# Kernel tuning notes

Measured on AMD Instinct MI355X. Metric: run time of the kernel, lower is better.

The kernel has to match this reference:

```python
import jax, jax.numpy as jnp
import numpy as np

B, T, D = 16, 4096, 256
CODEBOOK_SIZE = 1024
COMMITMENT = 1.0


def setup_inputs() -> dict:
    key = jax.random.key(0)
    kx, kc = jax.random.split(key)
    x = jax.random.normal(kx, (B, T, D), dtype=jnp.float32)
    codebook = jax.random.normal(kc, (CODEBOOK_SIZE, D), dtype=jnp.float32)
    return {"x": x, "codebook": codebook}


def reference(x, codebook):
    # x: [B, T, D] continuous latents; codebook: [K, D]
    flat = x.reshape(-1, x.shape[-1])  # [N, D]
    # does not affect argmin but is kept for faithfulness to torch.cdist-style math)
    x_sq = jnp.sum(flat * flat, axis=1, keepdims=True)            # [N, 1]
    c_sq = jnp.sum(codebook * codebook, axis=1)                   # [K]
    dist = x_sq - 2.0 * (flat @ codebook.T) + c_sq[None, :]       # [N, K]
    indices = jnp.argmin(dist, axis=1)                            # [N] int
    quantized = codebook[indices].reshape(x.shape)                # gather, [B, T, D]
    # commitment loss: encoder pulled toward (stopped) codes
    commit_loss = COMMITMENT * jnp.mean(
        (x - jax.lax.stop_gradient(quantized)) ** 2
    )
    # straight-through estimator
    out = x + jax.lax.stop_gradient(quantized - x)
    return out, indices.reshape(x.shape[:-1]), commit_loss
```

## Files before the change

kernel.cpp:

```cpp
#include <hip/hip_runtime.h>

#define N_TOK 65536
#define DIM   256
#define KCODE 1024

#define NTHREADS 256
#define TM 128
#define TN 128
#define BK 64
#define NCHUNK 8

#define REFINE_EPS 0.125f
#define TIE_THETA 1.0e-4

#define WS_CSQ_OFF   16
#define WS_IDX_OFF   2048
#define WS_PAIRS_OFF (WS_IDX_OFF + N_TOK)
#define WS_CBPK_OFF  (WS_PAIRS_OFF + N_TOK * NCHUNK * 4)

typedef float f32x4  __attribute__((ext_vector_type(4)));
typedef short bf16x8 __attribute__((ext_vector_type(8)));

__global__ void zero_loss_kernel(float* ws) {
    if (threadIdx.x == 0) ws[0] = 0.0f;
}

__global__ void rowsq_np_kernel(const float* __restrict__ m,
                                float* __restrict__ out, int rows) {
#pragma clang fp contract(off)
    int row = blockIdx.x * 16 + (threadIdx.x >> 4);
    int l   = threadIdx.x & 15;
    if (row >= rows) return;
    int h = l >> 3;
    int j = l & 7;
    const float* p = m + (size_t)row * DIM + h * 128 + j;
    float v = p[0];
    float r = v * v;
#pragma unroll
    for (int i = 1; i < 16; ++i) {
        float w  = p[i * 8];
        float w2 = w * w;
        r = r + w2;
    }
    float t = r + __shfl_xor(r, 1);
    t = t + __shfl_xor(t, 2);
    t = t + __shfl_xor(t, 4);
    t = t + __shfl_xor(t, 8);
    if (l == 0) out[row] = t;
}

__device__ __forceinline__ void ins2(float d, int idx,
                                     float& d1, int& i1, float& d2, int& i2) {
    if (d < d1 || (d == d1 && idx < i1)) {
        d2 = d1; i2 = i1; d1 = d; i1 = idx;
    } else if ((d < d2 || (d == d2 && idx < i2)) && idx != i1) {
        d2 = d; i2 = idx;
    }
}

__device__ __forceinline__ void f2bf_split(float v, short& hi, short& lo) {
    unsigned u = __float_as_uint(v);
    unsigned r = (u + 0x7fffu + ((u >> 16) & 1u)) >> 16;
    hi = (short)r;
    float hf = __uint_as_float(r << 16);
    float lf = v - hf;
    unsigned u2 = __float_as_uint(lf);
    unsigned r2 = (u2 + 0x7fffu + ((u2 >> 16) & 1u)) >> 16;
    lo = (short)r2;
}

__global__ void convert_pack_kernel(const float* __restrict__ src,
                                    unsigned short* __restrict__ dst,
                                    int nquads) {
    for (int i = blockIdx.x * blockDim.x + threadIdx.x; i < nquads;
         i += gridDim.x * blockDim.x) {
        int row = i >> 6;
        int kq  = i & 63;
        float4 v = reinterpret_cast<const float4*>(src)[i];
        short h0, l0, h1, l1, h2, l2, h3, l3;
        f2bf_split(v.x, h0, l0); f2bf_split(v.y, h1, l1);
        f2bf_split(v.z, h2, l2); f2bf_split(v.w, h3, l3);
        *reinterpret_cast<short4*>(dst + (size_t)row * 512 + kq * 4) =
            make_short4(h0, h1, h2, h3);
        *reinterpret_cast<short4*>(dst + (size_t)row * 512 + 256 + kq * 4) =
            make_short4(l0, l1, l2, l3);
    }
}

__device__ __forceinline__ void gload_lds16(const unsigned short* g, unsigned short* lds) {
    __builtin_amdgcn_global_load_lds(
        (const __attribute__((address_space(1))) unsigned int*)g,
        (__attribute__((address_space(3))) unsigned int*)lds, 16, 0, 0);
}

__launch_bounds__(NTHREADS, 2)
__global__ void vq_main_kernel(const unsigned short* __restrict__ xpk,
                               const unsigned short* __restrict__ cbpk,
                               const float* __restrict__ csq,
                               float4* __restrict__ pairs) {
    __shared__ __align__(16) unsigned short shbuf[2][TM * BK + TN * BK];

    const int tid  = threadIdx.x;
    const int w    = tid >> 6;
    const int wy   = w >> 1;
    const int wx   = w & 1;
    const int lane = tid & 63;
    const int lm   = lane & 15;
    const int q    = lane >> 4;

    const int bx     = blockIdx.x;
    const int jj     = bx >> 3;
    const int grp    = (bx & 7) + ((jj >> 3) << 3);
    const int cchunk = jj & 7;
    const int tok0   = grp * TM;
    const int code0  = cchunk * TN;

    const int row_off = lane >> 3;
    const int slot    = lane & 7;
    const int kq      = slot ^ row_off;

    float cs_reg[4];
#pragma unroll
    for (int ni = 0; ni < 4; ++ni)
        cs_reg[ni] = csq[code0 + wx * 64 + ni * 16 + lm];

    f32x4 acc[4][4];
#pragma unroll
    for (int mi = 0; mi < 4; ++mi)
#pragma unroll
        for (int ni = 0; ni < 4; ++ni)
            acc[mi][ni] = (f32x4){0.f, 0.f, 0.f, 0.f};

    auto stage = [&](int p, int s) {
        const int seg = s >> 2;
        const int k0  = (s & 3) * BK;
        const int sa  = (seg == 2) ? 256 : 0;
        const int sb  = (seg == 1) ? 256 : 0;
        unsigned short* At = &shbuf[p][0];
        unsigned short* Bt = &shbuf[p][TM * BK];
#pragma unroll
        for (int inst = 0; inst < 4; ++inst) {
            int rbase = w * 32 + inst * 8;
            const unsigned short* ga =
                xpk + (size_t)(tok0 + rbase + row_off) * 512 + sa + k0 + kq * 8;
            gload_lds16(ga, &At[rbase * BK]);
            const unsigned short* gb =
                cbpk + (size_t)(code0 + rbase + row_off) * 512 + sb + k0 + kq * 8;
            gload_lds16(gb, &Bt[rbase * BK]);
        }
    };

    stage(0, 0);
    __syncthreads();

    int p = 0;
#pragma unroll 1
    for (int s = 0; s < 12; ++s) {
        if (s < 11) stage(p ^ 1, s + 1);

        const unsigned short* At = &shbuf[p][0];
        const unsigned short* Bt = &shbuf[p][TM * BK];
#pragma unroll
        for (int t = 0; t < 2; ++t) {
            bf16x8 af[4], bf[4];
#pragma unroll
            for (int mi = 0; mi < 4; ++mi) {
                int r = wy * 64 + mi * 16 + lm;
                af[mi] = *reinterpret_cast<const bf16x8*>(
                    &At[r * BK + (((t * 4 + q) ^ (r & 7)) * 8)]);
            }
#pragma unroll
            for (int ni = 0; ni < 4; ++ni) {
                int r = wx * 64 + ni * 16 + lm;
                bf[ni] = *reinterpret_cast<const bf16x8*>(
                    &Bt[r * BK + (((t * 4 + q) ^ (r & 7)) * 8)]);
            }
#pragma unroll
            for (int mi = 0; mi < 4; ++mi)
#pragma unroll
                for (int ni = 0; ni < 4; ++ni)
                    acc[mi][ni] = __builtin_amdgcn_mfma_f32_16x16x32_bf16(
                        af[mi], bf[ni], acc[mi][ni], 0, 0, 0);
        }

        __syncthreads();
        p ^= 1;
    }

    float4 (*pairs_sh)[2] = reinterpret_cast<float4(*)[2]>(&shbuf[0][0]);

#pragma unroll
    for (int mi = 0; mi < 4; ++mi) {
#pragma unroll
        for (int r = 0; r < 4; ++r) {
            int row_local = wy * 64 + mi * 16 + q * 4 + r;
            float l1 = 3.4e38f, l2 = 3.4e38f;
            int   j1 = 0x7fffffff, j2 = 0x7fffffff;
#pragma unroll
            for (int ni = 0; ni < 4; ++ni) {
                float d = cs_reg[ni] - 2.0f * acc[mi][ni][r];
                ins2(d, code0 + wx * 64 + ni * 16 + lm, l1, j1, l2, j2);
            }
#pragma unroll
            for (int m = 1; m < 16; m <<= 1) {
                float o1 = __shfl_xor(l1, m);
                int   p1 = __shfl_xor(j1, m);
                float o2 = __shfl_xor(l2, m);
                int   p2 = __shfl_xor(j2, m);
                ins2(o1, p1, l1, j1, l2, j2);
                ins2(o2, p2, l1, j1, l2, j2);
            }
            if (lm == 0) {
                float4 pr;
                pr.x = l1; pr.y = l2;
                pr.z = __int_as_float(j1); pr.w = __int_as_float(j2);
                pairs_sh[row_local][wx] = pr;
            }
        }
    }
    __syncthreads();
    if (tid < TM) {
        float4 pa = pairs_sh[tid][0];
        float4 pb = pairs_sh[tid][1];
        float d1 = pa.x, d2 = pa.y;
        int   i1 = __float_as_int(pa.z), i2 = __float_as_int(pa.w);
        ins2(pb.x, __float_as_int(pb.z), d1, i1, d2, i2);
        ins2(pb.y, __float_as_int(pb.w), d1, i1, d2, i2);
        float4 pr;
        pr.x = d1; pr.y = d2;
        pr.z = __int_as_float(i1); pr.w = __int_as_float(i2);
        pairs[(size_t)(tok0 + tid) * NCHUNK + cchunk] = pr;
    }
}

__global__ void merge_refine_kernel(const float* __restrict__ x,
                                    const float* __restrict__ cb,
                                    const float4* __restrict__ pairs,
                                    int* __restrict__ idx_out) {
    int t = blockIdx.x * 256 + threadIdx.x;
    if (t >= N_TOK) return;
    float4 p0 = pairs[(size_t)t * NCHUNK];
    float d1 = p0.x, d2 = p0.y;
    int   i1 = __float_as_int(p0.z), i2 = __float_as_int(p0.w);
#pragma unroll
    for (int c = 1; c < NCHUNK; ++c) {
        float4 p = pairs[(size_t)t * NCHUNK + c];
        ins2(p.x, __float_as_int(p.z), d1, i1, d2, i2);
        ins2(p.y, __float_as_int(p.w), d1, i1, d2, i2);
    }

    int pick = i1;
    if (d2 - d1 < REFINE_EPS) {
        const float* xr = x + (size_t)t * DIM;
        const float* c1 = cb + (size_t)i1 * DIM;
        const float* c2 = cb + (size_t)i2 * DIM;
        double sA = 0.0, dA = 0.0, sB = 0.0, dB = 0.0;
        for (int k = 0; k < DIM; ++k) {
            double xv = (double)xr[k];
            double a  = (double)c1[k];
            double b  = (double)c2[k];
            sA += a * a; dA += xv * a;
            sB += b * b; dB += xv * b;
        }
        double DA  = sA - 2.0 * dA;
        double DB  = sB - 2.0 * dB;
        double gap = DB - DA;
        if (gap > TIE_THETA)       pick = i1;
        else if (gap < -TIE_THETA) pick = i2;
        else                       pick = (i1 < i2) ? i1 : i2;
    }
    idx_out[t] = pick;
}

__launch_bounds__(NTHREADS)
__global__ void output_kernel(const float* __restrict__ x,
                              const float* __restrict__ cb,
                              const int* __restrict__ idx,
                              float* __restrict__ out_q,
                              float* __restrict__ out_idx,
                              float* __restrict__ loss_ws) {
    __shared__ int   sh_idx[TM];
    __shared__ float wsum[4];
    const int tid  = threadIdx.x;
    const int tok0 = blockIdx.x * TM;

    if (tid < TM) sh_idx[tid] = idx[tok0 + tid];
    __syncthreads();

    float lsum = 0.0f;
    for (int t = 0; t < TM; ++t) {
        int code = sh_idx[t];
        float qv = cb[(size_t)code * DIM + tid];
        float xv = x[(size_t)(tok0 + t) * DIM + tid];
        out_q[(size_t)(tok0 + t) * DIM + tid] = xv + (qv - xv);
        float df = xv - qv;
        lsum = fmaf(df, df, lsum);
    }
    if (tid < TM) out_idx[tok0 + tid] = (float)sh_idx[tid];

#pragma unroll
    for (int off = 1; off < 64; off <<= 1) lsum += __shfl_xor(lsum, off);
    if ((tid & 63) == 0) wsum[tid >> 6] = lsum;
    __syncthreads();
    if (tid == 0) atomicAdd(loss_ws, (wsum[0] + wsum[1]) + (wsum[2] + wsum[3]));
}

__global__ void finalize_kernel(const float* ws, float* out_loss) {
    if (threadIdx.x == 0) out_loss[0] = ws[0] * (1.0f / 16777216.0f);
}

extern "C" void kernel_launch(void* const* d_in, const int* in_sizes, int n_in,
                              void* d_out, int out_size, void* d_ws, size_t ws_size,
                              hipStream_t stream) {
    const float* x  = (const float*)d_in[0];
    const float* cb = (const float*)d_in[1];

    float* out      = (float*)d_out;
    float* out_q    = out;
    float* out_idx  = out + (size_t)N_TOK * DIM;
    float* out_loss = out_idx + N_TOK;

    float*  ws    = (float*)d_ws;
    float*  csq   = ws + WS_CSQ_OFF;
    int*    idx   = (int*)(ws + WS_IDX_OFF);
    float4* pairs = (float4*)(ws + WS_PAIRS_OFF);
    unsigned short* cbpk = (unsigned short*)(ws + WS_CBPK_OFF);
    unsigned short* xpk  = (unsigned short*)out_q;

    zero_loss_kernel<<<1, 64, 0, stream>>>(ws);
    rowsq_np_kernel<<<KCODE / 16, 256, 0, stream>>>(cb, csq, KCODE);
    convert_pack_kernel<<<4096, 256, 0, stream>>>(x, xpk, N_TOK * (DIM / 4));
    convert_pack_kernel<<<256, 256, 0, stream>>>(cb, cbpk, KCODE * (DIM / 4));
    vq_main_kernel<<<(N_TOK / TM) * NCHUNK, NTHREADS, 0, stream>>>(xpk, cbpk, csq, pairs);
    merge_refine_kernel<<<N_TOK / 256, 256, 0, stream>>>(x, cb, pairs, idx);
    output_kernel<<<N_TOK / TM, NTHREADS, 0, stream>>>(x, cb, idx, out_q, out_idx, ws);
    finalize_kernel<<<1, 64, 0, stream>>>(ws, out_loss);
}
```

Before: 917.5 us.

## Pre-tile packed bf16 operands into swizzled k-chunks and halve LDS tile depth

The pack kernel now writes x and codebook as contiguous pre-swizzled 128x32 tiles (hi and lo halves in separate chunks), so each GEMM stage is a few fully contiguous 16-byte global-to-LDS loads. BK drops from 64 to 32 with 24 stages, shrinking LDS per block, and the launch bound rises to 5 blocks per CU for more occupancy. LDS fragment offsets are precomputed outside the loop. In exchange there are twice as many barriers per block and less MFMA work between syncs.

Result: faster. 803.3 us (-12.4%).

```diff
diff --git a/kernel.cpp b/kernel.cpp
--- a/kernel.cpp
+++ b/kernel.cpp
@@ -7,8 +7,9 @@
 #define NTHREADS 256
 #define TM 128
 #define TN 128
-#define BK 64
+#define BK 32
 #define NCHUNK 8
+#define NSTAGE 24
 
 #define REFINE_EPS 0.125f
 #define TIE_THETA 1.0e-4
@@ -20,6 +21,7 @@
 
 typedef float f32x4  __attribute__((ext_vector_type(4)));
 typedef short bf16x8 __attribute__((ext_vector_type(8)));
+typedef short s16x8  __attribute__((ext_vector_type(8)));
 
 __global__ void zero_loss_kernel(float* ws) {
     if (threadIdx.x == 0) ws[0] = 0.0f;
@@ -69,22 +71,34 @@
     lo = (short)r2;
 }
 
-__global__ void convert_pack_kernel(const float* __restrict__ src,
-                                    unsigned short* __restrict__ dst,
-                                    int nquads) {
-    for (int i = blockIdx.x * blockDim.x + threadIdx.x; i < nquads;
-         i += gridDim.x * blockDim.x) {
-        int row = i >> 6;
-        int kq  = i & 63;
-        float4 v = reinterpret_cast<const float4*>(src)[i];
-        short h0, l0, h1, l1, h2, l2, h3, l3;
-        f2bf_split(v.x, h0, l0); f2bf_split(v.y, h1, l1);
-        f2bf_split(v.z, h2, l2); f2bf_split(v.w, h3, l3);
-        *reinterpret_cast<short4*>(dst + (size_t)row * 512 + kq * 4) =
-            make_short4(h0, h1, h2, h3);
-        *reinterpret_cast<short4*>(dst + (size_t)row * 512 + 256 + kq * 4) =
-            make_short4(l0, l1, l2, l3);
-    }
+__global__ void pack_tiles_kernel(const float* __restrict__ src,
+                                  unsigned short* __restrict__ dst,
+                                  int total) {
+    int tid = blockIdx.x * blockDim.x + threadIdx.x;
+    if (tid >= total) return;
+    int s   = tid & 3;
+    int r   = (tid >> 2) & 127;
+    int kc  = (tid >> 9) & 7;
+    int g   = tid >> 12;
+    int oct = s ^ ((r >> 1) & 3);
+
+    const float4* xr = reinterpret_cast<const float4*>(
+        src + ((size_t)(g * 128 + r)) * DIM + kc * 32 + oct * 8);
+    float4 v0 = xr[0];
+    float4 v1 = xr[1];
+
+    float f[8] = {v0.x, v0.y, v0.z, v0.w, v1.x, v1.y, v1.z, v1.w};
+    s16x8 hv, lv;
+#pragma unroll
+    for (int i = 0; i < 8; ++i) {
+        short h, l;
+        f2bf_split(f[i], h, l);
+        hv[i] = h; lv[i] = l;
+    }
+    size_t base_hi = (((size_t)(g * 16 + kc) * 128 + r) << 5) + s * 8;
+    size_t base_lo = (((size_t)(g * 16 + 8 + kc) * 128 + r) << 5) + s * 8;
+    *reinterpret_cast<s16x8*>(dst + base_hi) = hv;
+    *reinterpret_cast<s16x8*>(dst + base_lo) = lv;
 }
 
 __device__ __forceinline__ void gload_lds16(const unsigned short* g, unsigned short* lds) {
@@ -93,12 +107,12 @@
         (__attribute__((address_space(3))) unsigned int*)lds, 16, 0, 0);
 }
 
-__launch_bounds__(NTHREADS, 2)
+__launch_bounds__(NTHREADS, 5)
 __global__ void vq_main_kernel(const unsigned short* __restrict__ xpk,
                                const unsigned short* __restrict__ cbpk,
                                const float* __restrict__ csq,
                                float4* __restrict__ pairs) {
-    __shared__ __align__(16) unsigned short shbuf[2][TM * BK + TN * BK];
+    __shared__ __align__(16) unsigned short shbuf[2][2 * TM * BK];
 
     const int tid  = threadIdx.x;
     const int w    = tid >> 6;
@@ -115,10 +129,6 @@
     const int tok0   = grp * TM;
     const int code0  = cchunk * TN;
 
-    const int row_off = lane >> 3;
-    const int slot    = lane & 7;
-    const int kq      = slot ^ row_off;
-
     float cs_reg[4];
 #pragma unroll
     for (int ni = 0; ni < 4; ++ni)
@@ -131,23 +141,32 @@
         for (int ni = 0; ni < 4; ++ni)
             acc[mi][ni] = (f32x4){0.f, 0.f, 0.f, 0.f};
 
+    int offA[4], offB[4];
+#pragma unroll
+    for (int mi = 0; mi < 4; ++mi) {
+        int r = wy * 64 + mi * 16 + lm;
+        offA[mi] = r * BK + ((q ^ ((r >> 1) & 3)) * 8);
+    }
+#pragma unroll
+    for (int ni = 0; ni < 4; ++ni) {
+        int r = wx * 64 + ni * 16 + lm;
+        offB[ni] = TM * BK + r * BK + ((q ^ ((r >> 1) & 3)) * 8);
+    }
+
+    const int lsrc = w * 1024 + lane * 8;
     auto stage = [&](int p, int s) {
-        const int seg = s >> 2;
-        const int k0  = (s & 3) * BK;
-        const int sa  = (seg == 2) ? 256 : 0;
-        const int sb  = (seg == 1) ? 256 : 0;
-        unsigned short* At = &shbuf[p][0];
-        unsigned short* Bt = &shbuf[p][TM * BK];
-#pragma unroll
-        for (int inst = 0; inst < 4; ++inst) {
-            int rbase = w * 32 + inst * 8;
-            const unsigned short* ga =
-                xpk + (size_t)(tok0 + rbase + row_off) * 512 + sa + k0 + kq * 8;
-            gload_lds16(ga, &At[rbase * BK]);
-            const unsigned short* gb =
-                cbpk + (size_t)(code0 + rbase + row_off) * 512 + sb + k0 + kq * 8;
-            gload_lds16(gb, &Bt[rbase * BK]);
-        }
+        const int seg = s >> 3;
+        const int kc  = s & 7;
+        const int pa  = (seg == 2) ? 8 : 0;
+        const int pb  = (seg == 1) ? 8 : 0;
+        const unsigned short* ga = xpk  + (((size_t)(grp    * 16 + pa + kc)) << 12) + lsrc;
+        const unsigned short* gb = cbpk + (((size_t)(cchunk * 16 + pb + kc)) << 12) + lsrc;
+        unsigned short* At = &shbuf[p][w * 1024];
+        unsigned short* Bt = &shbuf[p][TM * BK + w * 1024];
+        gload_lds16(ga,       At);
+        gload_lds16(ga + 512, At + 512);
+        gload_lds16(gb,       Bt);
+        gload_lds16(gb + 512, Bt + 512);
     };
 
     stage(0, 0);
@@ -155,33 +174,23 @@
 
     int p = 0;
 #pragma unroll 1
-    for (int s = 0; s < 12; ++s) {
-        if (s < 11) stage(p ^ 1, s + 1);
-
-        const unsigned short* At = &shbuf[p][0];
-        const unsigned short* Bt = &shbuf[p][TM * BK];
-#pragma unroll
-        for (int t = 0; t < 2; ++t) {
-            bf16x8 af[4], bf[4];
-#pragma unroll
-            for (int mi = 0; mi < 4; ++mi) {
-                int r = wy * 64 + mi * 16 + lm;
-                af[mi] = *reinterpret_cast<const bf16x8*>(
-                    &At[r * BK + (((t * 4 + q) ^ (r & 7)) * 8)]);
-            }
-#pragma unroll
-            for (int ni = 0; ni < 4; ++ni) {
-                int r = wx * 64 + ni * 16 + lm;
-                bf[ni] = *reinterpret_cast<const bf16x8*>(
-                    &Bt[r * BK + (((t * 4 + q) ^ (r & 7)) * 8)]);
-            }
-#pragma unroll
-            for (int mi = 0; mi < 4; ++mi)
-#pragma unroll
-                for (int ni = 0; ni < 4; ++ni)
-                    acc[mi][ni] = __builtin_amdgcn_mfma_f32_16x16x32_bf16(
-                        af[mi], bf[ni], acc[mi][ni], 0, 0, 0);
-        }
+    for (int s = 0; s < NSTAGE; ++s) {
+        if (s < NSTAGE - 1) stage(p ^ 1, s + 1);
+
+        const unsigned short* buf = &shbuf[p][0];
+        bf16x8 af[4], bf[4];
+#pragma unroll
+        for (int mi = 0; mi < 4; ++mi)
+            af[mi] = *reinterpret_cast<const bf16x8*>(buf + offA[mi]);
+#pragma unroll
+        for (int ni = 0; ni < 4; ++ni)
+            bf[ni] = *reinterpret_cast<const bf16x8*>(buf + offB[ni]);
+#pragma unroll
+        for (int mi = 0; mi < 4; ++mi)
+#pragma unroll
+            for (int ni = 0; ni < 4; ++ni)
+                acc[mi][ni] = __builtin_amdgcn_mfma_f32_16x16x32_bf16(
+                    af[mi], bf[ni], acc[mi][ni], 0, 0, 0);
 
         __syncthreads();
         p ^= 1;
@@ -329,8 +338,8 @@
 
     zero_loss_kernel<<<1, 64, 0, stream>>>(ws);
     rowsq_np_kernel<<<KCODE / 16, 256, 0, stream>>>(cb, csq, KCODE);
-    convert_pack_kernel<<<4096, 256, 0, stream>>>(x, xpk, N_TOK * (DIM / 4));
-    convert_pack_kernel<<<256, 256, 0, stream>>>(cb, cbpk, KCODE * (DIM / 4));
+    pack_tiles_kernel<<<(N_TOK * 32) / 256, 256, 0, stream>>>(x, xpk, N_TOK * 32);
+    pack_tiles_kernel<<<(KCODE * 32) / 256, 256, 0, stream>>>(cb, cbpk, KCODE * 32);
     vq_main_kernel<<<(N_TOK / TM) * NCHUNK, NTHREADS, 0, stream>>>(xpk, cbpk, csq, pairs);
     merge_refine_kernel<<<N_TOK / 256, 256, 0, stream>>>(x, cb, pairs, idx);
     output_kernel<<<N_TOK / TM, NTHREADS, 0, stream>>>(x, cb, idx, out_q, out_idx, ws);
```
